# Kernel optimization log

Measured on AMD Instinct MI355X. Metric: run time of the kernel, lower is better.

## Reference

```python
import jax, jax.numpy as jnp
import numpy as np

FEATS = 64
POS = 3
EDGE_ATTR = 4
M_DIM = 16
N_LAYERS = 3
EDGE_IN = 2 * FEATS + EDGE_ATTR + 1  # 133


def setup_inputs() -> dict:
    key = jax.random.key(0)
    ks = jax.random.split(key, 20)
    N, E = 50000, 800000
    x = jax.random.normal(ks[0], (N, FEATS + POS), dtype=jnp.float32)
    edge_index = jax.random.randint(ks[1], (2, E), 0, N, dtype=jnp.int64)
    edge_attr = jax.random.normal(ks[2], (E, EDGE_ATTR), dtype=jnp.float32)
    s = 0.02
    L = N_LAYERS
    inp = {
        "x": x, "edge_index": edge_index, "edge_attr": edge_attr,
        # edge_mlp: Linear(EDGE_IN, 2*EDGE_IN) -> SiLU -> Linear(2*EDGE_IN, M_DIM) -> SiLU
        "edge_w1": jax.random.normal(ks[3], (L, EDGE_IN, 2 * EDGE_IN), dtype=jnp.float32) * s,
        "edge_b1": jnp.zeros((L, 2 * EDGE_IN), dtype=jnp.float32),
        "edge_w2": jax.random.normal(ks[4], (L, 2 * EDGE_IN, M_DIM), dtype=jnp.float32) * s,
        "edge_b2": jnp.zeros((L, M_DIM), dtype=jnp.float32),
        # coors_mlp: Linear(M, 4M) -> SiLU -> Linear(4M, 1)
        "coors_w1": jax.random.normal(ks[5], (L, M_DIM, 4 * M_DIM), dtype=jnp.float32) * s,
        "coors_b1": jnp.zeros((L, 4 * M_DIM), dtype=jnp.float32),
        "coors_w2": jax.random.normal(ks[6], (L, 4 * M_DIM, 1), dtype=jnp.float32) * s,
        "coors_b2": jnp.zeros((L, 1), dtype=jnp.float32),
        # node_mlp: Linear(FEATS+M, 2*FEATS) -> SiLU -> Linear(2*FEATS, FEATS)
        "node_w1": jax.random.normal(ks[7], (L, FEATS + M_DIM, 2 * FEATS), dtype=jnp.float32) * s,
        "node_b1": jnp.zeros((L, 2 * FEATS), dtype=jnp.float32),
        "node_w2": jax.random.normal(ks[8], (L, 2 * FEATS, FEATS), dtype=jnp.float32) * s,
        "node_b2": jnp.zeros((L, FEATS), dtype=jnp.float32),
    }
    return inp


def _egnn_layer(x, edge_index, edge_attr,
                ew1, eb1, ew2, eb2, cw1, cb1, cw2, cb2, nw1, nb1, nw2, nb2):
    N = x.shape[0]
    feats, coors = x[:, :FEATS], x[:, FEATS:]
    src, dst = edge_index[0], edge_index[1]
    rel_coors = coors[src] - coors[dst]                       # [E, 3]
    rel_dist = jnp.sum(rel_coors ** 2, axis=-1, keepdims=True)  # [E, 1]
    ea = jnp.concatenate([edge_attr, rel_dist], axis=-1)      # [E, EDGE_ATTR+1]
    # PyG default flow source_to_target: x_i = x[dst], x_j = x[src]
    edge_in = jnp.concatenate([feats[dst], feats[src], ea], axis=-1)  # [E, EDGE_IN]
    h = jax.nn.silu(edge_in @ ew1 + eb1)
    m_ij = jax.nn.silu(h @ ew2 + eb2)                         # [E, M_DIM]
    coor_w = jax.nn.silu(m_ij @ cw1 + cb1) @ cw2 + cb2        # [E, 1]
    # aggregate (default 'add') over destination nodes
    m_i = jax.ops.segment_sum(m_ij, dst, num_segments=N)      # [N, M_DIM]
    coor_wi = jax.ops.segment_sum(coor_w, dst, num_segments=N)  # [N, 1]
    coor_ri = jax.ops.segment_sum(rel_coors, dst, num_segments=N)  # [N, 3]
    coors_out = coors + coor_wi * coor_ri
    node_in = jnp.concatenate([feats, m_i], axis=-1)
    hidden = jax.nn.silu(node_in @ nw1 + nb1) @ nw2 + nb2
    hidden_out = hidden + feats
    return jnp.concatenate([hidden_out, coors_out], axis=-1)


def reference(x, edge_index, edge_attr,
              edge_w1, edge_b1, edge_w2, edge_b2,
              coors_w1, coors_b1, coors_w2, coors_b2,
              node_w1, node_b1, node_w2, node_b2):
    for l in range(N_LAYERS):
        x = _egnn_layer(x, edge_index, edge_attr,
                        edge_w1[l], edge_b1[l], edge_w2[l], edge_b2[l],
                        coors_w1[l], coors_b1[l], coors_w2[l], coors_b2[l],
                        node_w1[l], node_b1[l], node_w2[l], node_b2[l])
    return x
```

## Files before the change

kernel.cpp:

```cpp
#include <hip/hip_runtime.h>
#include <hip/hip_bf16.h>

#define XDIM 67
#define EIN_D 133
#define H1 266
#define KP 160
#define KP_E 168
#define JP 320
#define JP_H 328
#define MSTR 40
#define EPB 48

typedef __attribute__((ext_vector_type(8))) short bf16x8;
typedef __attribute__((ext_vector_type(4))) float f32x4;
typedef __attribute__((ext_vector_type(2))) float f32x2;
typedef __attribute__((ext_vector_type(2))) __bf16 b16x2;

__device__ __forceinline__ float silu_f(float x) { return x / (1.f + __expf(-x)); }

__device__ __forceinline__ unsigned short bf16_rne(float f) {
    unsigned int u = __float_as_uint(f);
    u += 0x7fffu + ((u >> 16) & 1u);
    return (unsigned short)(u >> 16);
}
__device__ __forceinline__ float bf16_to_f(unsigned short h) {
    return __uint_as_float(((unsigned int)h) << 16);
}
__device__ __forceinline__ unsigned int packbf2(float a, float b) {
    b16x2 c = __builtin_convertvector((f32x2){a, b}, b16x2);
    unsigned int u; __builtin_memcpy(&u, &c, 4); return u;
}

__global__ void copy_zero_kernel(const float* __restrict__ src, float* __restrict__ dst,
                                 int n, float* __restrict__ z, int nz) {
    int n4 = n >> 2, nz4 = nz >> 2;
    const float4* s4 = (const float4*)src;
    float4* d4 = (float4*)dst;
    float4* z4 = (float4*)z;
    for (int i = blockIdx.x * blockDim.x + threadIdx.x; i < n4; i += gridDim.x * blockDim.x)
        d4[i] = s4[i];
    for (int i = blockIdx.x * blockDim.x + threadIdx.x; i < nz4; i += gridDim.x * blockDim.x)
        z4[i] = make_float4(0.f, 0.f, 0.f, 0.f);
    if (blockIdx.x == 0 && threadIdx.x == 0) {
        for (int i = n4 * 4; i < n; ++i) dst[i] = src[i];
        for (int i = nz4 * 4; i < nz; ++i) z[i] = 0.f;
    }
}

__global__ void prep_w1t(const float* __restrict__ ew1, unsigned short* __restrict__ whi,
                         unsigned short* __restrict__ wlo) {
    int idx = blockIdx.x * 256 + threadIdx.x;
    if (idx >= 3 * JP * KP) return;
    int l = idx / (JP * KP);
    int rem = idx - l * JP * KP;
    int j = rem / KP, k = rem - (rem / KP) * KP;
    float w = (j < H1 && k < EIN_D) ? ew1[((size_t)l * EIN_D + k) * H1 + j] : 0.f;
    unsigned short h = bf16_rne(w);
    whi[idx] = h;
    wlo[idx] = bf16_rne(w - bf16_to_f(h));
}

__global__ void prep_w2t(const float* __restrict__ ew2, unsigned short* __restrict__ w2tg) {
    int idx = blockIdx.x * 256 + threadIdx.x;
    if (idx >= 3 * 16 * JP_H) return;
    int l = idx / (16 * JP_H);
    int rem = idx - l * 16 * JP_H;
    int c = rem / JP_H, j = rem - (rem / JP_H) * JP_H;
    float w = (j < H1) ? ew2[((size_t)l * H1 + j) * 16 + c] : 0.f;
    unsigned short h = bf16_rne(w);
    w2tg[((size_t)l * 2 + 0) * 16 * JP_H + c * JP_H + j] = h;
    w2tg[((size_t)l * 2 + 1) * 16 * JP_H + c * JP_H + j] = bf16_rne(w - bf16_to_f(h));
}

__global__ void prep_b1(const float* __restrict__ b1, float* __restrict__ b1p) {
    int idx = blockIdx.x * 256 + threadIdx.x;
    if (idx >= 3 * JP) return;
    int l = idx / JP, j = idx - (idx / JP) * JP;
    b1p[idx] = (j < H1) ? b1[l * H1 + j] : 0.f;
}

__global__ void prep_cw1t(const float* __restrict__ cw1, unsigned short* __restrict__ cw1t) {
    int idx = blockIdx.x * 256 + threadIdx.x;
    if (idx >= 3 * 64 * 32) return;
    int l = idx / (64 * 32);
    int rem = idx - l * 64 * 32;
    int j = rem >> 5, c = rem & 31;
    cw1t[idx] = (c < 16) ? bf16_rne(cw1[(size_t)l * 16 * 64 + c * 64 + j]) : (unsigned short)0;
}

__global__ __launch_bounds__(256, 4) void edge_kernel(
    const float* __restrict__ x,
    const int* __restrict__ eidx,
    const float* __restrict__ eattr,
    const unsigned short* __restrict__ w1hi,
    const unsigned short* __restrict__ w1lo,
    const float* __restrict__ b1p,
    const unsigned short* __restrict__ w2tg,
    const float* __restrict__ b2,
    const unsigned short* __restrict__ cw1t,
    const float* __restrict__ cb1,
    const float* __restrict__ cw2, const float* __restrict__ cb2,
    float* __restrict__ m_i, float* __restrict__ cri, float* __restrict__ cwi,
    int E, int N)
{
    __shared__ __align__(16) unsigned short uA[2 * EPB * KP_E];
    __shared__ __align__(16) unsigned short mij_bf[EPB * MSTR];
    __shared__ float relc[EPB][4];
    __shared__ int dstl[EPB], srcl[EPB];

    unsigned short* ein_hi = uA;
    unsigned short* ein_lo = uA + EPB * KP_E;
    unsigned short* h_hi   = uA;

    const int tid = threadIdx.x;
    const int lane = tid & 63;
    const int w = tid >> 6;
    const int ge0 = blockIdx.x * EPB;
    const int r16 = lane & 15, g4 = lane >> 4;

    if (tid < EPB) {
        int e = tid, ge = ge0 + e;
        if (ge < E) {
            int s = eidx[ge];
            int d = eidx[E + ge];
            dstl[e] = d; srcl[e] = s;
            const float* xs = x + (size_t)s * XDIM;
            const float* xd = x + (size_t)d * XDIM;
            float r0 = xs[64] - xd[64], r1 = xs[65] - xd[65], r2 = xs[66] - xd[66];
            relc[e][0] = r0; relc[e][1] = r1; relc[e][2] = r2;
            float dist = r0 * r0 + r1 * r1 + r2 * r2;
            unsigned short hh = bf16_rne(dist);
            ein_hi[e * KP_E + 132] = hh;
            ein_lo[e * KP_E + 132] = bf16_rne(dist - bf16_to_f(hh));
        } else {
            dstl[e] = 0; srcl[e] = 0;
            relc[e][0] = relc[e][1] = relc[e][2] = 0.f;
            ein_hi[e * KP_E + 132] = 0;
            ein_lo[e * KP_E + 132] = 0;
        }
    }
    if (tid >= 64) {
        int t = tid - 64;
        int e = t >> 2, c = t & 3, ge = ge0 + e;
        float a = (ge < E) ? eattr[(size_t)ge * 4 + c] : 0.f;
        unsigned short hh = bf16_rne(a);
        ein_hi[e * KP_E + 128 + c] = hh;
        ein_lo[e * KP_E + 128 + c] = bf16_rne(a - bf16_to_f(hh));
    }
    for (int t = tid; t < EPB * 27; t += 256) {
        int e = t / 27, c = 133 + (t - (t / 27) * 27);
        ein_hi[e * KP_E + c] = 0;
        ein_lo[e * KP_E + c] = 0;
    }
    if (tid < 192) {
        int e = tid >> 2, q = tid & 3;
        uint2 zz; zz.x = 0u; zz.y = 0u;
        *(uint2*)&mij_bf[e * MSTR + 16 + q * 4] = zz;
    }
    __syncthreads();

    {
        const int rquad = g4;
        const int c0 = r16 * 4;
        const int ebase = w * 12;
#pragma unroll
        for (int q = 0; q < 3; ++q) {
            int er = ebase + q * 4 + rquad;
            const float* xdr = x + (size_t)dstl[er] * XDIM;
            const float* xsr = x + (size_t)srcl[er] * XDIM;
            float d0 = xdr[c0], d1 = xdr[c0 + 1], d2 = xdr[c0 + 2], d3 = xdr[c0 + 3];
            float s0 = xsr[c0], s1 = xsr[c0 + 1], s2 = xsr[c0 + 2], s3 = xsr[c0 + 3];
            unsigned int dh01 = packbf2(d0, d1), dh23 = packbf2(d2, d3);
            unsigned int sh01 = packbf2(s0, s1), sh23 = packbf2(s2, s3);
            float dl0 = d0 - __uint_as_float(dh01 << 16);
            float dl1 = d1 - __uint_as_float(dh01 & 0xffff0000u);
            float dl2 = d2 - __uint_as_float(dh23 << 16);
            float dl3 = d3 - __uint_as_float(dh23 & 0xffff0000u);
            float sl0 = s0 - __uint_as_float(sh01 << 16);
            float sl1 = s1 - __uint_as_float(sh01 & 0xffff0000u);
            float sl2 = s2 - __uint_as_float(sh23 << 16);
            float sl3 = s3 - __uint_as_float(sh23 & 0xffff0000u);
            uint2 vh, vl;
            vh.x = dh01; vh.y = dh23;
            vl.x = packbf2(dl0, dl1); vl.y = packbf2(dl2, dl3);
            *(uint2*)&ein_hi[er * KP_E + c0] = vh;
            *(uint2*)&ein_lo[er * KP_E + c0] = vl;
            vh.x = sh01; vh.y = sh23;
            vl.x = packbf2(sl0, sl1); vl.y = packbf2(sl2, sl3);
            *(uint2*)&ein_hi[er * KP_E + 64 + c0] = vh;
            *(uint2*)&ein_lo[er * KP_E + 64 + c0] = vl;
        }
    }
    __syncthreads();

    const int jt0 = w * 5;

    f32x4 acc[5][3];
#pragma unroll
    for (int a = 0; a < 5; ++a)
#pragma unroll
        for (int b = 0; b < 3; ++b) acc[a][b] = (f32x4){0.f, 0.f, 0.f, 0.f};

#pragma unroll
    for (int kk = 0; kk < 5; ++kk) {
        const int ko = kk * 32 + g4 * 8;
        bf16x8 ah[3], al[3];
#pragma unroll
        for (int et = 0; et < 3; ++et) {
            ah[et] = *(const bf16x8*)&ein_hi[(et * 16 + r16) * KP_E + ko];
            al[et] = *(const bf16x8*)&ein_lo[(et * 16 + r16) * KP_E + ko];
        }
#pragma unroll
        for (int j5 = 0; j5 < 5; ++j5) {
            const size_t wo = (size_t)((jt0 + j5) * 16 + r16) * KP + ko;
            bf16x8 bh = *(const bf16x8*)&w1hi[wo];
            bf16x8 bl = *(const bf16x8*)&w1lo[wo];
#pragma unroll
            for (int et = 0; et < 3; ++et) {
                acc[j5][et] = __builtin_amdgcn_mfma_f32_16x16x32_bf16(bh, ah[et], acc[j5][et], 0, 0, 0);
                acc[j5][et] = __builtin_amdgcn_mfma_f32_16x16x32_bf16(bl, ah[et], acc[j5][et], 0, 0, 0);
                acc[j5][et] = __builtin_amdgcn_mfma_f32_16x16x32_bf16(bh, al[et], acc[j5][et], 0, 0, 0);
            }
        }
    }

    float4 b1v[5];
#pragma unroll
    for (int j5 = 0; j5 < 5; ++j5)
        b1v[j5] = *(const float4*)&b1p[(jt0 + j5) * 16 + g4 * 4];

    __syncthreads();

#pragma unroll
    for (int j5 = 0; j5 < 5; ++j5) {
#pragma unroll
        for (int et = 0; et < 3; ++et) {
            f32x4 a = acc[j5][et];
            float h0 = silu_f(a[0] + b1v[j5].x);
            float h1 = silu_f(a[1] + b1v[j5].y);
            float h2 = silu_f(a[2] + b1v[j5].z);
            float h3 = silu_f(a[3] + b1v[j5].w);
            uint2 uu;
            uu.x = packbf2(h0, h1);
            uu.y = packbf2(h2, h3);
            *(uint2*)&h_hi[(et * 16 + r16) * JP_H + (jt0 + j5) * 16 + g4 * 4] = uu;
        }
    }
    __syncthreads();

    if (w < 3) {
        f32x4 acc2 = (f32x4){0.f, 0.f, 0.f, 0.f};
        const unsigned short* hrow = &h_hi[(w * 16 + r16) * JP_H];
        const unsigned short* w2h = &w2tg[(size_t)r16 * JP_H];
        const unsigned short* w2l = &w2tg[(size_t)(16 + r16) * JP_H];
#pragma unroll
        for (int kk = 0; kk < 10; ++kk) {
            const int ko = kk * 32 + g4 * 8;
            bf16x8 hf = *(const bf16x8*)&hrow[ko];
            bf16x8 wh = *(const bf16x8*)&w2h[ko];
            bf16x8 wl = *(const bf16x8*)&w2l[ko];
            acc2 = __builtin_amdgcn_mfma_f32_16x16x32_bf16(hf, wh, acc2, 0, 0, 0);
            acc2 = __builtin_amdgcn_mfma_f32_16x16x32_bf16(hf, wl, acc2, 0, 0, 0);
        }
        float b2v = b2[r16];
#pragma unroll
        for (int r = 0; r < 4; ++r) {
            int e = w * 16 + g4 * 4 + r;
            float m = silu_f(acc2[r] + b2v);
            mij_bf[e * MSTR + r16] = bf16_rne(m);
            if (ge0 + e < E) atomicAdd(&m_i[(size_t)dstl[e] * 16 + r16], m);
        }
    }
    __syncthreads();

    if (w < 3) {
        bf16x8 afrag = *(const bf16x8*)&mij_bf[(w * 16 + r16) * MSTR + g4 * 8];
        f32x4 cacc[4];
#pragma unroll
        for (int jt = 0; jt < 4; ++jt) {
            bf16x8 bfrag = *(const bf16x8*)&cw1t[(jt * 16 + r16) * 32 + g4 * 8];
            cacc[jt] = __builtin_amdgcn_mfma_f32_16x16x32_bf16(afrag, bfrag,
                        (f32x4){0.f, 0.f, 0.f, 0.f}, 0, 0, 0);
        }
        float pw0 = 0.f, pw1 = 0.f, pw2 = 0.f, pw3 = 0.f;
#pragma unroll
        for (int jt = 0; jt < 4; ++jt) {
            float cb = cb1[jt * 16 + r16];
            float cw = cw2[jt * 16 + r16];
            pw0 += silu_f(cacc[jt][0] + cb) * cw;
            pw1 += silu_f(cacc[jt][1] + cb) * cw;
            pw2 += silu_f(cacc[jt][2] + cb) * cw;
            pw3 += silu_f(cacc[jt][3] + cb) * cw;
        }
#pragma unroll
        for (int s = 1; s < 16; s <<= 1) {
            pw0 += __shfl_xor(pw0, s, 16);
            pw1 += __shfl_xor(pw1, s, 16);
            pw2 += __shfl_xor(pw2, s, 16);
            pw3 += __shfl_xor(pw3, s, 16);
        }
        if (r16 == 0) {
            float cb2v = cb2[0];
            int e = w * 16 + g4 * 4;
            relc[e + 0][3] = pw0 + cb2v;
            relc[e + 1][3] = pw1 + cb2v;
            relc[e + 2][3] = pw2 + cb2v;
            relc[e + 3][3] = pw3 + cb2v;
        }
    }
    __syncthreads();

    if (tid < EPB * 4) {
        int e = tid >> 2, c = tid & 3;
        if (ge0 + e < E) {
            int d = dstl[e];
            if (c < 3) atomicAdd(&cri[(size_t)d * 3 + c], relc[e][c]);
            else       atomicAdd(&cwi[d], relc[e][3]);
        }
    }
}

__global__ __launch_bounds__(256) void node_kernel(
    const float* xin,
    float* __restrict__ m_i,
    float* __restrict__ cri,
    float* __restrict__ cwi,
    const float* __restrict__ nw1, const float* __restrict__ nb1,
    const float* __restrict__ nw2, const float* __restrict__ nb2,
    float* xout, int N)
{
    __shared__ __align__(16) float nin[2][80];
    __shared__ __align__(16) float hid[2][128];
    const int half = threadIdx.x >> 7, r = threadIdx.x & 127;
    const int n = blockIdx.x * 2 + half;
    const bool on = (n < N);

    if (on) {
        if (r < 64)      nin[half][r] = xin[(size_t)n * XDIM + r];
        else if (r < 80) nin[half][r] = m_i[(size_t)n * 16 + (r - 64)];
    }
    __syncthreads();
    if (on) {
        float h = nb1[r];
#pragma unroll
        for (int k = 0; k < 80; k += 4) {
            float4 a = *(const float4*)&nin[half][k];
            h += a.x * nw1[k * 128 + r] + a.y * nw1[(k + 1) * 128 + r]
               + a.z * nw1[(k + 2) * 128 + r] + a.w * nw1[(k + 3) * 128 + r];
        }
        hid[half][r] = silu_f(h);
    }
    __syncthreads();
    if (on) {
        if (r < 64) {
            float o = nb2[r];
#pragma unroll
            for (int k = 0; k < 128; k += 4) {
                float4 a = *(const float4*)&hid[half][k];
                o += a.x * nw2[k * 64 + r] + a.y * nw2[(k + 1) * 64 + r]
                   + a.z * nw2[(k + 2) * 64 + r] + a.w * nw2[(k + 3) * 64 + r];
            }
            xout[(size_t)n * XDIM + r] = o + nin[half][r];
        } else if (r < 67) {
            int c = r - 64;
            xout[(size_t)n * XDIM + r] =
                xin[(size_t)n * XDIM + r] + cwi[n] * cri[(size_t)n * 3 + c];
        }
    }
    __syncthreads();
    if (on) {
        if (r < 16)      m_i[(size_t)n * 16 + r] = 0.f;
        else if (r < 19) cri[(size_t)n * 3 + (r - 16)] = 0.f;
        else if (r == 19) cwi[n] = 0.f;
    }
}

extern "C" void kernel_launch(void* const* d_in, const int* in_sizes, int n_in,
                              void* d_out, int out_size, void* d_ws, size_t ws_size,
                              hipStream_t stream) {
    const float* x     = (const float*)d_in[0];
    const int*   eidx  = (const int*)d_in[1];
    const float* eattr = (const float*)d_in[2];
    const float* ew1   = (const float*)d_in[3];
    const float* eb1   = (const float*)d_in[4];
    const float* ew2   = (const float*)d_in[5];
    const float* eb2   = (const float*)d_in[6];
    const float* cw1   = (const float*)d_in[7];
    const float* cb1   = (const float*)d_in[8];
    const float* cw2   = (const float*)d_in[9];
    const float* cb2   = (const float*)d_in[10];
    const float* nw1   = (const float*)d_in[11];
    const float* nb1   = (const float*)d_in[12];
    const float* nw2   = (const float*)d_in[13];
    const float* nb2   = (const float*)d_in[14];

    const int N = in_sizes[0] / XDIM;
    const int E = in_sizes[1] / 2;

    float* acc  = (float*)d_ws;
    float* m_i  = acc;
    float* cri  = acc + (size_t)N * 16;
    float* cwi  = acc + (size_t)N * 19;
    float* b1p  = acc + (size_t)N * 20;
    unsigned short* w1hi = (unsigned short*)(b1p + (size_t)3 * JP);
    unsigned short* w1lo = w1hi + (size_t)3 * JP * KP;
    unsigned short* w2tg = w1lo + (size_t)3 * JP * KP;
    unsigned short* cw1t = w2tg + (size_t)3 * 2 * 16 * JP_H;

    float* xwork = (float*)d_out;

    copy_zero_kernel<<<2048, 256, 0, stream>>>(x, xwork, N * XDIM, acc, N * 20);
    prep_w1t<<<(3 * JP * KP + 255) / 256, 256, 0, stream>>>(ew1, w1hi, w1lo);
    prep_w2t<<<(3 * 16 * JP_H + 255) / 256, 256, 0, stream>>>(ew2, w2tg);
    prep_b1<<<(3 * JP + 255) / 256, 256, 0, stream>>>(eb1, b1p);
    prep_cw1t<<<(3 * 64 * 32 + 255) / 256, 256, 0, stream>>>(cw1, cw1t);

    for (int l = 0; l < 3; ++l) {
        edge_kernel<<<(E + EPB - 1) / EPB, 256, 0, stream>>>(
            xwork, eidx, eattr,
            w1hi + (size_t)l * JP * KP, w1lo + (size_t)l * JP * KP,
            b1p + (size_t)l * JP,
            w2tg + (size_t)l * 2 * 16 * JP_H,
            eb2 + (size_t)l * 16,
            cw1t + (size_t)l * 64 * 32,
            cb1 + (size_t)l * 64,
            cw2 + (size_t)l * 64, cb2 + l,
            m_i, cri, cwi, E, N);
        node_kernel<<<(N + 1) / 2, 256, 0, stream>>>(
            xwork, m_i, cri, cwi,
            nw1 + (size_t)l * 80 * 128, nb1 + (size_t)l * 128,
            nw2 + (size_t)l * 128 * 64, nb2 + (size_t)l * 64,
            xwork, N);
    }
}
```

Before: 1.807 ms.

## Prefetch edge feature gathers early, add MFMA priority, split node-MLP accumulators

Each thread now loads its edge indices and source/destination feature rows into registers at kernel entry, before the shared-memory setup. This removes one barrier and lets the random gathers overlap with the other setup work. The MFMA loop is wrapped in s_setprio to raise wave priority, silu uses a hardware reciprocal instead of a divide, and the node MLP dot products use four independent accumulators to shorten dependency chains. The early register loads raise register pressure and may hurt occupancy, and the reciprocal changes rounding slightly.

```diff
diff --git a/kernel.cpp b/kernel.cpp
--- a/kernel.cpp
+++ b/kernel.cpp
@@ -16,7 +16,9 @@
 typedef __attribute__((ext_vector_type(2))) float f32x2;
 typedef __attribute__((ext_vector_type(2))) __bf16 b16x2;
 
-__device__ __forceinline__ float silu_f(float x) { return x / (1.f + __expf(-x)); }
+__device__ __forceinline__ float silu_f(float x) {
+    return x * __builtin_amdgcn_rcpf(1.f + __expf(-x));
+}
 
 __device__ __forceinline__ unsigned short bf16_rne(float f) {
     unsigned int u = __float_as_uint(f);
@@ -86,6 +88,30 @@
     int rem = idx - l * 64 * 32;
     int j = rem >> 5, c = rem & 31;
     cw1t[idx] = (c < 16) ? bf16_rne(cw1[(size_t)l * 16 * 64 + c * 64 + j]) : (unsigned short)0;
+}
+
+__device__ __forceinline__ void store_feats(unsigned short* __restrict__ ein_hi,
+                                            unsigned short* __restrict__ ein_lo,
+                                            int er, int c0, const float* v) {
+    unsigned int dh01 = packbf2(v[0], v[1]), dh23 = packbf2(v[2], v[3]);
+    unsigned int sh01 = packbf2(v[4], v[5]), sh23 = packbf2(v[6], v[7]);
+    float dl0 = v[0] - __uint_as_float(dh01 << 16);
+    float dl1 = v[1] - __uint_as_float(dh01 & 0xffff0000u);
+    float dl2 = v[2] - __uint_as_float(dh23 << 16);
+    float dl3 = v[3] - __uint_as_float(dh23 & 0xffff0000u);
+    float sl0 = v[4] - __uint_as_float(sh01 << 16);
+    float sl1 = v[5] - __uint_as_float(sh01 & 0xffff0000u);
+    float sl2 = v[6] - __uint_as_float(sh23 << 16);
+    float sl3 = v[7] - __uint_as_float(sh23 & 0xffff0000u);
+    uint2 u;
+    u.x = dh01; u.y = dh23;
+    *(uint2*)&ein_hi[er * KP_E + c0] = u;
+    u.x = packbf2(dl0, dl1); u.y = packbf2(dl2, dl3);
+    *(uint2*)&ein_lo[er * KP_E + c0] = u;
+    u.x = sh01; u.y = sh23;
+    *(uint2*)&ein_hi[er * KP_E + 64 + c0] = u;
+    u.x = packbf2(sl0, sl1); u.y = packbf2(sl2, sl3);
+    *(uint2*)&ein_lo[er * KP_E + 64 + c0] = u;
 }
 
 __global__ __launch_bounds__(256, 4) void edge_kernel(
@@ -106,7 +132,7 @@
     __shared__ __align__(16) unsigned short uA[2 * EPB * KP_E];
     __shared__ __align__(16) unsigned short mij_bf[EPB * MSTR];
     __shared__ float relc[EPB][4];
-    __shared__ int dstl[EPB], srcl[EPB];
+    __shared__ int dstl[EPB];
 
     unsigned short* ein_hi = uA;
     unsigned short* ein_lo = uA + EPB * KP_E;
@@ -118,12 +144,29 @@
     const int ge0 = blockIdx.x * EPB;
     const int r16 = lane & 15, g4 = lane >> 4;
 
+    const int c0 = r16 * 4;
+    const int erA = w * 12 + g4, erB = erA + 4, erC = erA + 8;
+    const int geA = ge0 + erA, geB = ge0 + erB, geC = ge0 + erC;
+    const int sA = (geA < E) ? eidx[geA] : 0, dA = (geA < E) ? eidx[E + geA] : 0;
+    const int sB = (geB < E) ? eidx[geB] : 0, dB = (geB < E) ? eidx[E + geB] : 0;
+    const int sC = (geC < E) ? eidx[geC] : 0, dC = (geC < E) ? eidx[E + geC] : 0;
+    float vA[8], vB[8], vC[8];
+    {
+        const float* p;
+        p = x + (size_t)dA * XDIM + c0; vA[0] = p[0]; vA[1] = p[1]; vA[2] = p[2]; vA[3] = p[3];
+        p = x + (size_t)sA * XDIM + c0; vA[4] = p[0]; vA[5] = p[1]; vA[6] = p[2]; vA[7] = p[3];
+        p = x + (size_t)dB * XDIM + c0; vB[0] = p[0]; vB[1] = p[1]; vB[2] = p[2]; vB[3] = p[3];
+        p = x + (size_t)sB * XDIM + c0; vB[4] = p[0]; vB[5] = p[1]; vB[6] = p[2]; vB[7] = p[3];
+        p = x + (size_t)dC * XDIM + c0; vC[0] = p[0]; vC[1] = p[1]; vC[2] = p[2]; vC[3] = p[3];
+        p = x + (size_t)sC * XDIM + c0; vC[4] = p[0]; vC[5] = p[1]; vC[6] = p[2]; vC[7] = p[3];
+    }
+
     if (tid < EPB) {
         int e = tid, ge = ge0 + e;
         if (ge < E) {
             int s = eidx[ge];
             int d = eidx[E + ge];
-            dstl[e] = d; srcl[e] = s;
+            dstl[e] = d;
             const float* xs = x + (size_t)s * XDIM;
             const float* xd = x + (size_t)d * XDIM;
             float r0 = xs[64] - xd[64], r1 = xs[65] - xd[65], r2 = xs[66] - xd[66];
@@ -133,7 +176,7 @@
             ein_hi[e * KP_E + 132] = hh;
             ein_lo[e * KP_E + 132] = bf16_rne(dist - bf16_to_f(hh));
         } else {
-            dstl[e] = 0; srcl[e] = 0;
+            dstl[e] = 0;
             relc[e][0] = relc[e][1] = relc[e][2] = 0.f;
             ein_hi[e * KP_E + 132] = 0;
             ein_lo[e * KP_E + 132] = 0;
@@ -157,40 +200,10 @@
         uint2 zz; zz.x = 0u; zz.y = 0u;
         *(uint2*)&mij_bf[e * MSTR + 16 + q * 4] = zz;
     }
-    __syncthreads();
-
-    {
-        const int rquad = g4;
-        const int c0 = r16 * 4;
-        const int ebase = w * 12;
-#pragma unroll
-        for (int q = 0; q < 3; ++q) {
-            int er = ebase + q * 4 + rquad;
-            const float* xdr = x + (size_t)dstl[er] * XDIM;
-            const float* xsr = x + (size_t)srcl[er] * XDIM;
-            float d0 = xdr[c0], d1 = xdr[c0 + 1], d2 = xdr[c0 + 2], d3 = xdr[c0 + 3];
-            float s0 = xsr[c0], s1 = xsr[c0 + 1], s2 = xsr[c0 + 2], s3 = xsr[c0 + 3];
-            unsigned int dh01 = packbf2(d0, d1), dh23 = packbf2(d2, d3);
-            unsigned int sh01 = packbf2(s0, s1), sh23 = packbf2(s2, s3);
-            float dl0 = d0 - __uint_as_float(dh01 << 16);
-            float dl1 = d1 - __uint_as_float(dh01 & 0xffff0000u);
-            float dl2 = d2 - __uint_as_float(dh23 << 16);
-            float dl3 = d3 - __uint_as_float(dh23 & 0xffff0000u);
-            float sl0 = s0 - __uint_as_float(sh01 << 16);
-            float sl1 = s1 - __uint_as_float(sh01 & 0xffff0000u);
-            float sl2 = s2 - __uint_as_float(sh23 << 16);
-            float sl3 = s3 - __uint_as_float(sh23 & 0xffff0000u);
-            uint2 vh, vl;
-            vh.x = dh01; vh.y = dh23;
-            vl.x = packbf2(dl0, dl1); vl.y = packbf2(dl2, dl3);
-            *(uint2*)&ein_hi[er * KP_E + c0] = vh;
-            *(uint2*)&ein_lo[er * KP_E + c0] = vl;
-            vh.x = sh01; vh.y = sh23;
-            vl.x = packbf2(sl0, sl1); vl.y = packbf2(sl2, sl3);
-            *(uint2*)&ein_hi[er * KP_E + 64 + c0] = vh;
-            *(uint2*)&ein_lo[er * KP_E + 64 + c0] = vl;
-        }
-    }
+
+    store_feats(ein_hi, ein_lo, erA, c0, vA);
+    store_feats(ein_hi, ein_lo, erB, c0, vB);
+    store_feats(ein_hi, ein_lo, erC, c0, vC);
     __syncthreads();
 
     const int jt0 = w * 5;
@@ -201,6 +214,7 @@
 #pragma unroll
         for (int b = 0; b < 3; ++b) acc[a][b] = (f32x4){0.f, 0.f, 0.f, 0.f};
 
+    __builtin_amdgcn_s_setprio(1);
 #pragma unroll
     for (int kk = 0; kk < 5; ++kk) {
         const int ko = kk * 32 + g4 * 8;
@@ -223,6 +237,7 @@
             }
         }
     }
+    __builtin_amdgcn_s_setprio(0);
 
     float4 b1v[5];
 #pragma unroll
@@ -341,26 +356,44 @@
     }
     __syncthreads();
     if (on) {
-        float h = nb1[r];
-#pragma unroll
-        for (int k = 0; k < 80; k += 4) {
-            float4 a = *(const float4*)&nin[half][k];
-            h += a.x * nw1[k * 128 + r] + a.y * nw1[(k + 1) * 128 + r]
-               + a.z * nw1[(k + 2) * 128 + r] + a.w * nw1[(k + 3) * 128 + r];
-        }
-        hid[half][r] = silu_f(h);
+        float p0 = 0.f, p1 = 0.f, p2 = 0.f, p3 = 0.f;
+#pragma unroll
+        for (int k = 0; k < 80; k += 16) {
+            float4 a0 = *(const float4*)&nin[half][k];
+            float4 a1 = *(const float4*)&nin[half][k + 4];
+            float4 a2 = *(const float4*)&nin[half][k + 8];
+            float4 a3 = *(const float4*)&nin[half][k + 12];
+            p0 += a0.x * nw1[(k + 0) * 128 + r] + a0.y * nw1[(k + 1) * 128 + r]
+                + a0.z * nw1[(k + 2) * 128 + r] + a0.w * nw1[(k + 3) * 128 + r];
+            p1 += a1.x * nw1[(k + 4) * 128 + r] + a1.y * nw1[(k + 5) * 128 + r]
+                + a1.z * nw1[(k + 6) * 128 + r] + a1.w * nw1[(k + 7) * 128 + r];
+            p2 += a2.x * nw1[(k + 8) * 128 + r] + a2.y * nw1[(k + 9) * 128 + r]
+                + a2.z * nw1[(k + 10) * 128 + r] + a2.w * nw1[(k + 11) * 128 + r];
+            p3 += a3.x * nw1[(k + 12) * 128 + r] + a3.y * nw1[(k + 13) * 128 + r]
+                + a3.z * nw1[(k + 14) * 128 + r] + a3.w * nw1[(k + 15) * 128 + r];
+        }
+        hid[half][r] = silu_f(nb1[r] + ((p0 + p1) + (p2 + p3)));
     }
     __syncthreads();
     if (on) {
         if (r < 64) {
-            float o = nb2[r];
-#pragma unroll
-            for (int k = 0; k < 128; k += 4) {
-                float4 a = *(const float4*)&hid[half][k];
-                o += a.x * nw2[k * 64 + r] + a.y * nw2[(k + 1) * 64 + r]
-                   + a.z * nw2[(k + 2) * 64 + r] + a.w * nw2[(k + 3) * 64 + r];
+            float p0 = 0.f, p1 = 0.f, p2 = 0.f, p3 = 0.f;
+#pragma unroll
+            for (int k = 0; k < 128; k += 16) {
+                float4 a0 = *(const float4*)&hid[half][k];
+                float4 a1 = *(const float4*)&hid[half][k + 4];
+                float4 a2 = *(const float4*)&hid[half][k + 8];
+                float4 a3 = *(const float4*)&hid[half][k + 12];
+                p0 += a0.x * nw2[(k + 0) * 64 + r] + a0.y * nw2[(k + 1) * 64 + r]
+                    + a0.z * nw2[(k + 2) * 64 + r] + a0.w * nw2[(k + 3) * 64 + r];
+                p1 += a1.x * nw2[(k + 4) * 64 + r] + a1.y * nw2[(k + 5) * 64 + r]
+                    + a1.z * nw2[(k + 6) * 64 + r] + a1.w * nw2[(k + 7) * 64 + r];
+                p2 += a2.x * nw2[(k + 8) * 64 + r] + a2.y * nw2[(k + 9) * 64 + r]
+                    + a2.z * nw2[(k + 10) * 64 + r] + a2.w * nw2[(k + 11) * 64 + r];
+                p3 += a3.x * nw2[(k + 12) * 64 + r] + a3.y * nw2[(k + 13) * 64 + r]
+                    + a3.z * nw2[(k + 14) * 64 + r] + a3.w * nw2[(k + 15) * 64 + r];
             }
-            xout[(size_t)n * XDIM + r] = o + nin[half][r];
+            xout[(size_t)n * XDIM + r] = nb2[r] + ((p0 + p1) + (p2 + p3)) + nin[half][r];
         } else if (r < 67) {
             int c = r - 64;
             xout[(size_t)n * XDIM + r] =
```

Result: faster. 1.761 ms (-2.6%).
